# Optimization experiments

Hardware: AMD Instinct MI355X
Metric: run time of the kernel (lower is better)

The kernel has to match this reference:

```python
import jax, jax.numpy as jnp
import numpy as np

D_MODEL = 1024
N_HEADS = 16
D_FF = 4096
WINDOW = 256
EPS = 1e-5


def setup_inputs() -> dict:
    key = jax.random.key(0)
    ks = jax.random.split(key, 12)
    B, T, C = 4, 1024, D_MODEL
    s = lambda fan: 1.0 / np.sqrt(fan)
    return {
        "x": jax.random.normal(ks[0], (B, T, C), jnp.float32),
        "Wqkv": jax.random.normal(ks[1], (3 * C, C), jnp.float32) * s(C),
        "bqkv": jnp.zeros((3 * C,), jnp.float32),
        "Wo": jax.random.normal(ks[2], (C, C), jnp.float32) * s(C),
        "bo": jnp.zeros((C,), jnp.float32),
        "W1": jax.random.normal(ks[3], (D_FF, C), jnp.float32) * s(C),
        "b1": jnp.zeros((D_FF,), jnp.float32),
        "W2": jax.random.normal(ks[4], (C, D_FF), jnp.float32) * s(D_FF),
        "b2": jnp.zeros((C,), jnp.float32),
        "g1": jnp.ones((C,), jnp.float32),
        "be1": jnp.zeros((C,), jnp.float32),
        "g2": jnp.ones((C,), jnp.float32),
        "be2": jnp.zeros((C,), jnp.float32),
    }


def _layernorm(x, g, b):
    mu = jnp.mean(x, axis=-1, keepdims=True)
    var = jnp.mean(jnp.square(x - mu), axis=-1, keepdims=True)
    return (x - mu) * jax.lax.rsqrt(var + EPS) * g + b


def reference(x, Wqkv, bqkv, Wo, bo, W1, b1, W2, b2, g1, be1, g2, be2):
    B, T, C = x.shape
    H, Dh = N_HEADS, C // N_HEADS
    # QKV projection (torch MultiheadAttention packed in_proj)
    qkv = jnp.einsum("btc,ec->bte", x, Wqkv) + bqkv  # [B,T,3C]
    q, k, v = jnp.split(qkv, 3, axis=-1)
    q = q.reshape(B, T, H, Dh).transpose(0, 2, 1, 3)  # [B,H,T,Dh]
    k = k.reshape(B, T, H, Dh).transpose(0, 2, 1, 3)
    v = v.reshape(B, T, H, Dh).transpose(0, 2, 1, 3)
    scores = jnp.einsum("bhqd,bhkd->bhqk", q, k) / jnp.sqrt(jnp.float32(Dh))
    # causal banded mask: key j visible to query i iff 0 <= i-j < WINDOW
    i = jnp.arange(T)[:, None]
    j = jnp.arange(T)[None, :]
    band = (j <= i) & (i - j < WINDOW)
    scores = jnp.where(band, scores, -jnp.inf)
    attn = jax.nn.softmax(scores, axis=-1)
    ctx = jnp.einsum("bhqk,bhkd->bhqd", attn, v)  # [B,H,T,Dh]
    ctx = ctx.transpose(0, 2, 1, 3).reshape(B, T, C)
    attn_out = jnp.einsum("btc,oc->bto", ctx, Wo) + bo
    x = _layernorm(x + attn_out, g1, be1)
    h = jax.nn.gelu(jnp.einsum("btc,fc->btf", x, W1) + b1, approximate=False)
    ffn_out = jnp.einsum("btf,cf->btc", h, W2) + b2
    return _layernorm(x + ffn_out, g2, be2)
```

## Files before the change

kernel.cpp:

```cpp
#include <hip/hip_runtime.h>
#include <hip/hip_bf16.h>

typedef __attribute__((ext_vector_type(4))) float floatx4;
typedef __attribute__((ext_vector_type(8))) short shortx8;

struct bf4 { __hip_bfloat16 h[4]; };
union U8 { shortx8 v; __hip_bfloat16 h[8]; };
union U4 { unsigned long long v; __hip_bfloat16 h[4]; };

__device__ __forceinline__ void async_copy16(const __hip_bfloat16* g, __hip_bfloat16* l) {
  __builtin_amdgcn_global_load_lds((__attribute__((address_space(1))) void*)g,
                                   (__attribute__((address_space(3))) void*)l,
                                   16, 0, 0);
}

__global__ __launch_bounds__(256) void cast_all_kernel(
    const float* __restrict__ s0, __hip_bfloat16* __restrict__ d0, int nb0,
    const float* __restrict__ s1, __hip_bfloat16* __restrict__ d1, int nb1,
    const float* __restrict__ s2, __hip_bfloat16* __restrict__ d2, int nb2,
    const float* __restrict__ s3, __hip_bfloat16* __restrict__ d3, int nb3,
    const float* __restrict__ s4, __hip_bfloat16* __restrict__ d4) {
  int b = blockIdx.x;
  const float* src; __hip_bfloat16* dst;
  if (b < nb0) { src = s0; dst = d0; }
  else { b -= nb0;
    if (b < nb1) { src = s1; dst = d1; }
    else { b -= nb1;
      if (b < nb2) { src = s2; dst = d2; }
      else { b -= nb2;
        if (b < nb3) { src = s3; dst = d3; }
        else { b -= nb3; src = s4; dst = d4; }
      }
    }
  }
  const int i = b * 256 + threadIdx.x;
  const float4 v = ((const float4*)src)[i];
  bf4 o4;
  o4.h[0] = __float2bfloat16(v.x);
  o4.h[1] = __float2bfloat16(v.y);
  o4.h[2] = __float2bfloat16(v.z);
  o4.h[3] = __float2bfloat16(v.w);
  *(bf4*)(dst + (size_t)i * 4) = o4;
}

#define G5_VM(n)   asm volatile("s_waitcnt vmcnt(" #n ")" ::: "memory")
#define G5_BAR()   asm volatile("s_barrier" ::: "memory")
#define G5_LGKM0() asm volatile("s_waitcnt lgkmcnt(0)" ::: "memory")
#define G5_SB()    __builtin_amdgcn_sched_barrier(0)

#define G5_STAGE(slot, koff)                                                   \
  async_copy16(Ag + (koff), &As[slot][tid * 8]);                               \
  async_copy16(Bg + (koff), &Bs[slot][tid * 8]);

#define G5_PHASE(slot, SOFF, DOSTG, VMW)                                       \
  {                                                                            \
    shortx8 fa[4], fb[4];                                                      \
    _Pragma("unroll")                                                          \
    for (int i_ = 0; i_ < 4; ++i_)                                             \
      fa[i_] = *(const shortx8*)&As[slot][ard + i_ * 512];                     \
    _Pragma("unroll")                                                          \
    for (int i_ = 0; i_ < 4; ++i_)                                             \
      fb[i_] = *(const shortx8*)&Bs[slot][brd + i_ * 512];                     \
    if (DOSTG) { G5_STAGE((((slot) + 3) & 3), SOFF) }                          \
    VMW;                                                                       \
    G5_BAR();                                                                  \
    G5_LGKM0(); G5_SB();                                                       \
    __builtin_amdgcn_s_setprio(1);                                             \
    _Pragma("unroll")                                                          \
    for (int mi_ = 0; mi_ < 4; ++mi_)                                          \
      _Pragma("unroll")                                                        \
      for (int ni_ = 0; ni_ < 4; ++ni_)                                        \
        acc[mi_][ni_] = __builtin_amdgcn_mfma_f32_16x16x32_bf16(               \
            fa[mi_], fb[ni_], acc[mi_][ni_], 0, 0, 0);                         \
    __builtin_amdgcn_s_setprio(0);                                             \
    G5_SB();                                                                   \
    G5_BAR();                                                                  \
  }

#define G5_KLOOP()                                                             \
  G5_STAGE(0, 0) G5_STAGE(1, 32) G5_STAGE(2, 64)                               \
  G5_VM(4); G5_BAR();                                                          \
  const int NITER = (NH - 4) >> 2;                                             \
  _Pragma("clang loop unroll(disable)")                                        \
  for (int it = 0; it < NITER; ++it) {                                         \
    G5_PHASE(0, 96,  true, G5_VM(4))                                           \
    G5_PHASE(1, 128, true, G5_VM(4))                                           \
    G5_PHASE(2, 160, true, G5_VM(4))                                           \
    G5_PHASE(3, 192, true, G5_VM(4))                                           \
    Ag += 128; Bg += 128;                                                      \
  }                                                                            \
  G5_PHASE(0, 96, true, G5_VM(4))                                              \
  G5_PHASE(1, 0, false, G5_VM(2))                                              \
  G5_PHASE(2, 0, false, G5_VM(0))                                              \
  G5_PHASE(3, 0, false, (void)0)

template<int EPI>
__global__ __launch_bounds__(1024, 4) void gemm256(
    const __hip_bfloat16* __restrict__ A,
    const __hip_bfloat16* __restrict__ B,
    const float* __restrict__ bias,
    __hip_bfloat16* __restrict__ outb,
    int M, int N, int K, int NT)
{
  __shared__ __align__(16) __hip_bfloat16 As[4][256 * 32];
  __shared__ __align__(16) __hip_bfloat16 Bs[4][256 * 32];
  const int tid  = threadIdx.x;
  const int lane = tid & 63;
  const int wave = tid >> 6;
  const int wr = wave >> 2;
  const int wc = wave & 3;
  const int fr = lane & 15;
  const int fq = lane >> 4;

  const int nwg = gridDim.x;
  const int cpx = nwg >> 3;
  const int swz = (blockIdx.x & 7) * cpx + (blockIdx.x >> 3);
  const int mt = swz / NT, nt = swz % NT;
  const long bm = (long)mt * 256, bn = (long)nt * 256;

  const int srow = tid >> 2;
  const int sch  = (tid & 3) ^ ((tid >> 3) & 3);
  const __hip_bfloat16* Ag = A + (bm + srow) * (size_t)K + sch * 8;
  const __hip_bfloat16* Bg = B + (bn + srow) * (size_t)K + sch * 8;

  const int swc = (fq ^ ((fr >> 1) & 3)) << 3;
  const int ard = (wr * 64 + fr) * 32 + swc;
  const int brd = (wc * 64 + fr) * 32 + swc;

  const floatx4 zero = {0.f, 0.f, 0.f, 0.f};
  floatx4 acc[4][4];
#pragma unroll
  for (int mi = 0; mi < 4; ++mi)
#pragma unroll
    for (int ni = 0; ni < 4; ++ni) acc[mi][ni] = zero;

  const int NH = K >> 5;
  G5_KLOOP()

#pragma unroll
  for (int mi = 0; mi < 4; ++mi) {
#pragma unroll
    for (int ni = 0; ni < 4; ++ni) {
      const long col = bn + wc * 64 + ni * 16 + fr;
      const float bv = bias[col];
#pragma unroll
      for (int r = 0; r < 4; ++r) {
        const long row = bm + wr * 64 + mi * 16 + fq * 4 + r;
        float v = acc[mi][ni][r] + bv;
        if (EPI == 1) {
          const float u = v + 0.044715f * v * v * v;
          v = v / (1.0f + __expf(-1.5957691216057308f * u));
        }
        outb[(size_t)row * N + col] = __float2bfloat16(v);
      }
    }
  }
}

__global__ __launch_bounds__(1024, 4) void gemm256_splitk(
    const __hip_bfloat16* __restrict__ A,
    const __hip_bfloat16* __restrict__ B,
    __hip_bfloat16* __restrict__ part,
    int M, int N, int K, int Klen, int NT, int TPS)
{
  __shared__ __align__(16) __hip_bfloat16 As[4][256 * 32];
  __shared__ __align__(16) __hip_bfloat16 Bs[4][256 * 32];
  const int tid  = threadIdx.x;
  const int lane = tid & 63;
  const int wave = tid >> 6;
  const int wr = wave >> 2;
  const int wc = wave & 3;
  const int fr = lane & 15;
  const int fq = lane >> 4;

  const int nwg = gridDim.x;
  const int cpx = nwg >> 3;
  const int swz = (blockIdx.x & 7) * cpx + (blockIdx.x >> 3);
  const int zt = swz / TPS;
  const int tile = swz % TPS;
  const int mt = tile / NT, nt = tile % NT;
  const long bm = (long)mt * 256, bn = (long)nt * 256;
  const int kstart = zt * Klen;

  const int srow = tid >> 2;
  const int sch  = (tid & 3) ^ ((tid >> 3) & 3);
  const __hip_bfloat16* Ag = A + (bm + srow) * (size_t)K + kstart + sch * 8;
  const __hip_bfloat16* Bg = B + (bn + srow) * (size_t)K + kstart + sch * 8;

  const int swc = (fq ^ ((fr >> 1) & 3)) << 3;
  const int ard = (wr * 64 + fr) * 32 + swc;
  const int brd = (wc * 64 + fr) * 32 + swc;

  const floatx4 zero = {0.f, 0.f, 0.f, 0.f};
  floatx4 acc[4][4];
#pragma unroll
  for (int mi = 0; mi < 4; ++mi)
#pragma unroll
    for (int ni = 0; ni < 4; ++ni) acc[mi][ni] = zero;

  const int NH = Klen >> 5;
  G5_KLOOP()

  __hip_bfloat16* outp = part + (size_t)zt * M * N;
#pragma unroll
  for (int mi = 0; mi < 4; ++mi) {
#pragma unroll
    for (int ni = 0; ni < 4; ++ni) {
      const long col = bn + wc * 64 + ni * 16 + fr;
#pragma unroll
      for (int r = 0; r < 4; ++r) {
        const long row = bm + wr * 64 + mi * 16 + fq * 4 + r;
        outp[(size_t)row * N + col] = __float2bfloat16(acc[mi][ni][r]);
      }
    }
  }
}

__global__ __launch_bounds__(256) void transpose_v_kernel(
    const __hip_bfloat16* __restrict__ qkv, __hip_bfloat16* __restrict__ vt)
{
  const int bh = blockIdx.y;
  const int tt = blockIdx.x;
  const int b = bh >> 4, h = bh & 15;
  __shared__ __hip_bfloat16 tile[64][65];
  const int tid = threadIdx.x;
  const int r = tid >> 2;
  const int c = (tid & 3) << 4;
  const __hip_bfloat16* src = qkv + (size_t)(b * 1024 + tt * 64 + r) * 3072 + 2048 + h * 64 + c;
  U8 u0, u1;
  u0.v = *(const shortx8*)src;
  u1.v = *(const shortx8*)(src + 8);
#pragma unroll
  for (int j = 0; j < 8; ++j) { tile[r][c + j] = u0.h[j]; tile[r][c + 8 + j] = u1.h[j]; }
  __syncthreads();
  U8 w0, w1;
#pragma unroll
  for (int j = 0; j < 8; ++j) { w0.h[j] = tile[c + j][r]; w1.h[j] = tile[c + 8 + j][r]; }
  __hip_bfloat16* dst = vt + ((size_t)bh * 64 + r) * 1024 + tt * 64 + c;
  *(shortx8*)dst       = w0.v;
  *(shortx8*)(dst + 8) = w1.v;
}

__global__ __launch_bounds__(256) void attn_kernel(
    const __hip_bfloat16* __restrict__ qkv,
    const __hip_bfloat16* __restrict__ vt,
    __hip_bfloat16* __restrict__ ctx)
{
  const int wave = threadIdx.x >> 6;
  const int lane = threadIdx.x & 63;
  const int gw = blockIdx.x * 4 + wave;
  const int qt = gw & 63;
  const int bh = gw >> 6;
  const int b = bh >> 4, h = bh & 15;
  const int fr = lane & 15, fq = lane >> 4;
  const int q0 = qt << 4;

  __shared__ __align__(16) __hip_bfloat16 Plds[4][16 * 32];
  __hip_bfloat16* Pw = Plds[wave];

  const __hip_bfloat16* qrow = qkv + (size_t)(b * 1024 + q0 + fr) * 3072 + h * 64;
  const shortx8 aq0 = *(const shortx8*)(qrow + fq * 8);
  const shortx8 aq1 = *(const shortx8*)(qrow + 32 + fq * 8);

  const float SC = 0.125f * 1.44269504088896f;
  float m_r[4] = {-1e30f, -1e30f, -1e30f, -1e30f};
  float l_r[4] = {0.f, 0.f, 0.f, 0.f};
  const floatx4 zero = {0.f, 0.f, 0.f, 0.f};
  floatx4 o[4];
#pragma unroll
  for (int nd = 0; nd < 4; ++nd) o[nd] = zero;

  const int kt0 = (q0 >= 255) ? ((q0 - 255) >> 5) : 0;
  const int kt1 = (q0 + 15) >> 5;
  for (int kt = kt0; kt <= kt1; ++kt) {
    const int kbase = kt << 5;
    const __hip_bfloat16* krow0 = qkv + (size_t)(b * 1024 + kbase + fr) * 3072 + 1024 + h * 64;
    const __hip_bfloat16* krow1 = krow0 + 16 * 3072;
    const shortx8 bk00 = *(const shortx8*)(krow0 + fq * 8);
    const shortx8 bk01 = *(const shortx8*)(krow0 + 32 + fq * 8);
    const shortx8 bk10 = *(const shortx8*)(krow1 + fq * 8);
    const shortx8 bk11 = *(const shortx8*)(krow1 + 32 + fq * 8);
    floatx4 s0 = zero, s1 = zero;
    s0 = __builtin_amdgcn_mfma_f32_16x16x32_bf16(aq0, bk00, s0, 0, 0, 0);
    s0 = __builtin_amdgcn_mfma_f32_16x16x32_bf16(aq1, bk01, s0, 0, 0, 0);
    s1 = __builtin_amdgcn_mfma_f32_16x16x32_bf16(aq0, bk10, s1, 0, 0, 0);
    s1 = __builtin_amdgcn_mfma_f32_16x16x32_bf16(aq1, bk11, s1, 0, 0, 0);
#pragma unroll
    for (int r = 0; r < 4; ++r) { s0[r] *= SC; s1[r] *= SC; }
    if (kbase + 31 > q0 || kbase < q0 - 240) {
#pragma unroll
      for (int r = 0; r < 4; ++r) {
        const int tq = q0 + fq * 4 + r;
        const int j0 = kbase + fr;
        const int j1 = j0 + 16;
        if (j0 > tq || j0 < tq - 255) s0[r] = -3e38f;
        if (j1 > tq || j1 < tq - 255) s1[r] = -3e38f;
      }
    }
#pragma unroll
    for (int r = 0; r < 4; ++r) {
      float vmax = fmaxf(s0[r], s1[r]);
      vmax = fmaxf(vmax, __shfl_xor(vmax, 1));
      vmax = fmaxf(vmax, __shfl_xor(vmax, 2));
      vmax = fmaxf(vmax, __shfl_xor(vmax, 4));
      vmax = fmaxf(vmax, __shfl_xor(vmax, 8));
      const float mnew = fmaxf(m_r[r], vmax);
      const float alpha = exp2f(m_r[r] - mnew);
      const float p0 = exp2f(s0[r] - mnew);
      const float p1 = exp2f(s1[r] - mnew);
      m_r[r] = mnew;
      float ps = p0 + p1;
      ps += __shfl_xor(ps, 1);
      ps += __shfl_xor(ps, 2);
      ps += __shfl_xor(ps, 4);
      ps += __shfl_xor(ps, 8);
      l_r[r] = l_r[r] * alpha + ps;
      o[0][r] *= alpha; o[1][r] *= alpha; o[2][r] *= alpha; o[3][r] *= alpha;
      Pw[(fq * 4 + r) * 32 + fr]      = __float2bfloat16(p0);
      Pw[(fq * 4 + r) * 32 + 16 + fr] = __float2bfloat16(p1);
    }
    asm volatile("s_waitcnt lgkmcnt(0)" ::: "memory");
    const shortx8 ap = *(const shortx8*)&Pw[fr * 32 + fq * 8];
#pragma unroll
    for (int nd = 0; nd < 4; ++nd) {
      const shortx8 bv = *(const shortx8*)&vt[((size_t)bh * 64 + nd * 16 + fr) * 1024 + kbase + fq * 8];
      o[nd] = __builtin_amdgcn_mfma_f32_16x16x32_bf16(ap, bv, o[nd], 0, 0, 0);
    }
    asm volatile("s_waitcnt lgkmcnt(0)" ::: "memory");
  }
#pragma unroll
  for (int nd = 0; nd < 4; ++nd)
#pragma unroll
    for (int r = 0; r < 4; ++r)
      ctx[(size_t)(b * 1024 + q0 + fq * 4 + r) * 1024 + h * 64 + nd * 16 + fr] =
          __float2bfloat16(o[nd][r] / l_r[r]);
}

template<int S, int WB>
__global__ __launch_bounds__(256) void ln_sum_kernel(
    const __hip_bfloat16* __restrict__ part,
    const float* __restrict__ resid,
    const float* __restrict__ bias,
    const float* __restrict__ g, const float* __restrict__ be,
    float* __restrict__ outf, __hip_bfloat16* __restrict__ outb)
{
  const int row = blockIdx.x;
  const int tid = threadIdx.x;
  const size_t base = (size_t)row * 1024;
  float4 v = ((const float4*)(resid + base))[tid];
  const float4 bv = ((const float4*)bias)[tid];
  v.x += bv.x; v.y += bv.y; v.z += bv.z; v.w += bv.w;
#pragma unroll
  for (int s = 0; s < S; ++s) {
    U4 p;
    p.v = *(const unsigned long long*)&part[(size_t)s * 4096 * 1024 + base + tid * 4];
    v.x += __bfloat162float(p.h[0]);
    v.y += __bfloat162float(p.h[1]);
    v.z += __bfloat162float(p.h[2]);
    v.w += __bfloat162float(p.h[3]);
  }
  float sm = v.x + v.y + v.z + v.w;
  float ss = v.x * v.x + v.y * v.y + v.z * v.z + v.w * v.w;
#pragma unroll
  for (int off = 1; off < 64; off <<= 1) {
    sm += __shfl_xor(sm, off);
    ss += __shfl_xor(ss, off);
  }
  __shared__ float red[8];
  if ((tid & 63) == 0) { red[tid >> 6] = sm; red[4 + (tid >> 6)] = ss; }
  __syncthreads();
  sm = red[0] + red[1] + red[2] + red[3];
  ss = red[4] + red[5] + red[6] + red[7];
  const float mu = sm * (1.0f / 1024.0f);
  const float rs = rsqrtf(ss * (1.0f / 1024.0f) - mu * mu + 1e-5f);
  const float4 gg = ((const float4*)g)[tid];
  const float4 bb = ((const float4*)be)[tid];
  float4 y;
  y.x = (v.x - mu) * rs * gg.x + bb.x;
  y.y = (v.y - mu) * rs * gg.y + bb.y;
  y.z = (v.z - mu) * rs * gg.z + bb.z;
  y.w = (v.w - mu) * rs * gg.w + bb.w;
  ((float4*)(outf + base))[tid] = y;
  if (WB) {
    bf4 o4;
    o4.h[0] = __float2bfloat16(y.x);
    o4.h[1] = __float2bfloat16(y.y);
    o4.h[2] = __float2bfloat16(y.z);
    o4.h[3] = __float2bfloat16(y.w);
    *(bf4*)(outb + base + tid * 4) = o4;
  }
}

extern "C" void kernel_launch(void* const* d_in, const int* in_sizes, int n_in,
                              void* d_out, int out_size, void* d_ws, size_t ws_size,
                              hipStream_t stream) {
  const float* x    = (const float*)d_in[0];
  const float* Wqkv = (const float*)d_in[1];
  const float* bqkv = (const float*)d_in[2];
  const float* Wo   = (const float*)d_in[3];
  const float* bo   = (const float*)d_in[4];
  const float* W1   = (const float*)d_in[5];
  const float* b1   = (const float*)d_in[6];
  const float* W2   = (const float*)d_in[7];
  const float* b2   = (const float*)d_in[8];
  const float* g1   = (const float*)d_in[9];
  const float* be1  = (const float*)d_in[10];
  const float* g2   = (const float*)d_in[11];
  const float* be2  = (const float*)d_in[12];

  char* ws = (char*)d_ws;
  size_t off = 0;
  auto alloc = [&](size_t bytes) -> void* {
    void* p = ws + off;
    off += (bytes + 255) & ~(size_t)255;
    return p;
  };
  __hip_bfloat16* wqkvb = (__hip_bfloat16*)alloc(6291456);
  __hip_bfloat16* wob   = (__hip_bfloat16*)alloc(2097152);
  __hip_bfloat16* w1b   = (__hip_bfloat16*)alloc(8388608);
  __hip_bfloat16* w2b   = (__hip_bfloat16*)alloc(8388608);
  __hip_bfloat16* xb    = (__hip_bfloat16*)alloc(8388608);
  __hip_bfloat16* qkvb  = (__hip_bfloat16*)alloc(25165824);
  __hip_bfloat16* vtb   = (__hip_bfloat16*)alloc(8388608);
  __hip_bfloat16* ctxb  = (__hip_bfloat16*)alloc(8388608);
  __hip_bfloat16* part  = (__hip_bfloat16*)alloc(4u * 8388608);
  float*          x1f   = (float*)alloc(16777216);
  __hip_bfloat16* x1b   = (__hip_bfloat16*)alloc(8388608);
  __hip_bfloat16* hb    = (__hip_bfloat16*)alloc(33554432);
  (void)ws_size; (void)in_sizes; (void)n_in; (void)out_size;

  cast_all_kernel<<<16384, 256, 0, stream>>>(x, xb, 4096,
                                             Wqkv, wqkvb, 3072,
                                             Wo, wob, 1024,
                                             W1, w1b, 4096,
                                             W2, w2b);
  gemm256<0><<<192, 1024, 0, stream>>>(xb, wqkvb, bqkv, qkvb, 4096, 3072, 1024, 12);
  transpose_v_kernel<<<dim3(16, 64), 256, 0, stream>>>(qkvb, vtb);
  attn_kernel<<<1024, 256, 0, stream>>>(qkvb, vtb, ctxb);
  gemm256_splitk<<<256, 1024, 0, stream>>>(ctxb, wob, part, 4096, 1024, 1024, 256, 4, 64);
  ln_sum_kernel<4, 1><<<4096, 256, 0, stream>>>(part, x, bo, g1, be1, x1f, x1b);
  gemm256<1><<<256, 1024, 0, stream>>>(x1b, w1b, b1, hb, 4096, 4096, 1024, 16);
  gemm256_splitk<<<256, 1024, 0, stream>>>(hb, w2b, part, 4096, 1024, 4096, 1024, 4, 64);
  ln_sum_kernel<4, 0><<<4096, 256, 0, stream>>>(part, x1f, b2, g2, be2, (float*)d_out, nullptr);
}
```

Before: 324.3 us.

## Use five-slot LDS ring to drop second barrier per K-step in GEMM

Replaces the four-slot LDS pipeline, which needed two barriers per K-step and a manually unrolled phase macro, with a five-slot ring buffer. With the extra slot, a write into a slot cannot race with reads of that slot from the previous step, so the trailing barrier and the sched_barriers are removed. The loop becomes a generic runtime loop with rotating slot indices and tail vmcnt handling. LDS use rises from 128KB to 160KB per block, and the runtime slot arithmetic and branches add some scalar overhead.

```diff
diff --git a/kernel.cpp b/kernel.cpp
--- a/kernel.cpp
+++ b/kernel.cpp
@@ -43,56 +43,51 @@
   *(bf4*)(dst + (size_t)i * 4) = o4;
 }
 
-#define G5_VM(n)   asm volatile("s_waitcnt vmcnt(" #n ")" ::: "memory")
-#define G5_BAR()   asm volatile("s_barrier" ::: "memory")
-#define G5_LGKM0() asm volatile("s_waitcnt lgkmcnt(0)" ::: "memory")
-#define G5_SB()    __builtin_amdgcn_sched_barrier(0)
-
-#define G5_STAGE(slot, koff)                                                   \
-  async_copy16(Ag + (koff), &As[slot][tid * 8]);                               \
-  async_copy16(Bg + (koff), &Bs[slot][tid * 8]);
-
-#define G5_PHASE(slot, SOFF, DOSTG, VMW)                                       \
+#define G6_VM(n)   asm volatile("s_waitcnt vmcnt(" #n ")" ::: "memory")
+#define G6_BAR()   asm volatile("s_barrier" ::: "memory")
+#define G6_LGKM0() asm volatile("s_waitcnt lgkmcnt(0)" ::: "memory")
+
+#define G6_KLOOP()                                                             \
+  async_copy16(Ag,      &As[0 * 8192 + tid * 8]);                              \
+  async_copy16(Bg,      &Bs[0 * 8192 + tid * 8]);                              \
+  async_copy16(Ag + 32, &As[1 * 8192 + tid * 8]);                              \
+  async_copy16(Bg + 32, &Bs[1 * 8192 + tid * 8]);                              \
+  async_copy16(Ag + 64, &As[2 * 8192 + tid * 8]);                              \
+  async_copy16(Bg + 64, &Bs[2 * 8192 + tid * 8]);                              \
+  G6_VM(4); G6_BAR();                                                          \
   {                                                                            \
-    shortx8 fa[4], fb[4];                                                      \
-    _Pragma("unroll")                                                          \
-    for (int i_ = 0; i_ < 4; ++i_)                                             \
-      fa[i_] = *(const shortx8*)&As[slot][ard + i_ * 512];                     \
-    _Pragma("unroll")                                                          \
-    for (int i_ = 0; i_ < 4; ++i_)                                             \
-      fb[i_] = *(const shortx8*)&Bs[slot][brd + i_ * 512];                     \
-    if (DOSTG) { G5_STAGE((((slot) + 3) & 3), SOFF) }                          \
-    VMW;                                                                       \
-    G5_BAR();                                                                  \
-    G5_LGKM0(); G5_SB();                                                       \
-    __builtin_amdgcn_s_setprio(1);                                             \
-    _Pragma("unroll")                                                          \
-    for (int mi_ = 0; mi_ < 4; ++mi_)                                          \
+    int rs = 0, ws = 3, koff = 96;                                             \
+    for (int u = 0; u < NH; ++u) {                                             \
+      const __hip_bfloat16* Asl = As + rs * 8192;                              \
+      const __hip_bfloat16* Bsl = Bs + rs * 8192;                              \
+      shortx8 fa[4], fb[4];                                                    \
       _Pragma("unroll")                                                        \
-      for (int ni_ = 0; ni_ < 4; ++ni_)                                        \
-        acc[mi_][ni_] = __builtin_amdgcn_mfma_f32_16x16x32_bf16(               \
-            fa[mi_], fb[ni_], acc[mi_][ni_], 0, 0, 0);                         \
-    __builtin_amdgcn_s_setprio(0);                                             \
-    G5_SB();                                                                   \
-    G5_BAR();                                                                  \
-  }
-
-#define G5_KLOOP()                                                             \
-  G5_STAGE(0, 0) G5_STAGE(1, 32) G5_STAGE(2, 64)                               \
-  G5_VM(4); G5_BAR();                                                          \
-  const int NITER = (NH - 4) >> 2;                                             \
-  _Pragma("clang loop unroll(disable)")                                        \
-  for (int it = 0; it < NITER; ++it) {                                         \
-    G5_PHASE(0, 96,  true, G5_VM(4))                                           \
-    G5_PHASE(1, 128, true, G5_VM(4))                                           \
-    G5_PHASE(2, 160, true, G5_VM(4))                                           \
-    G5_PHASE(3, 192, true, G5_VM(4))                                           \
-    Ag += 128; Bg += 128;                                                      \
-  }                                                                            \
-  G5_PHASE(0, 96, true, G5_VM(4))                                              \
-  G5_PHASE(1, 0, false, G5_VM(2))                                              \
-  G5_PHASE(2, 0, false, G5_VM(0))                                              \
-  G5_PHASE(3, 0, false, (void)0)
+      for (int i_ = 0; i_ < 4; ++i_)                                           \
+        fa[i_] = *(const shortx8*)&Asl[ard + i_ * 512];                        \
+      _Pragma("unroll")                                                        \
+      for (int i_ = 0; i_ < 4; ++i_)                                           \
+        fb[i_] = *(const shortx8*)&Bsl[brd + i_ * 512];                        \
+      if (u + 3 < NH) {                                                        \
+        async_copy16(Ag + koff, &As[ws * 8192 + tid * 8]);                     \
+        async_copy16(Bg + koff, &Bs[ws * 8192 + tid * 8]);                     \
+        koff += 32;                                                            \
+        G6_VM(4);                                                              \
+      } else if (u + 2 < NH) { G6_VM(2); }                                     \
+      else if (u + 1 < NH)   { G6_VM(0); }                                     \
+      G6_BAR();                                                                \
+      G6_LGKM0();                                                              \
+      __builtin_amdgcn_s_setprio(1);                                           \
+      _Pragma("unroll")                                                        \
+      for (int mi_ = 0; mi_ < 4; ++mi_)                                        \
+        _Pragma("unroll")                                                      \
+        for (int ni_ = 0; ni_ < 4; ++ni_)                                      \
+          acc[mi_][ni_] = __builtin_amdgcn_mfma_f32_16x16x32_bf16(             \
+              fa[mi_], fb[ni_], acc[mi_][ni_], 0, 0, 0);                       \
+      __builtin_amdgcn_s_setprio(0);                                           \
+      rs = (rs == 4) ? 0 : rs + 1;                                             \
+      ws = (ws == 4) ? 0 : ws + 1;                                             \
+    }                                                                          \
+  }
 
 template<int EPI>
 __global__ __launch_bounds__(1024, 4) void gemm256(
@@ -102,8 +97,8 @@
     __hip_bfloat16* __restrict__ outb,
     int M, int N, int K, int NT)
 {
-  __shared__ __align__(16) __hip_bfloat16 As[4][256 * 32];
-  __shared__ __align__(16) __hip_bfloat16 Bs[4][256 * 32];
+  __shared__ __align__(16) __hip_bfloat16 As[5 * 8192];
+  __shared__ __align__(16) __hip_bfloat16 Bs[5 * 8192];
   const int tid  = threadIdx.x;
   const int lane = tid & 63;
   const int wave = tid >> 6;
@@ -135,7 +130,7 @@
     for (int ni = 0; ni < 4; ++ni) acc[mi][ni] = zero;
 
   const int NH = K >> 5;
-  G5_KLOOP()
+  G6_KLOOP()
 
 #pragma unroll
   for (int mi = 0; mi < 4; ++mi) {
@@ -163,8 +158,8 @@
     __hip_bfloat16* __restrict__ part,
     int M, int N, int K, int Klen, int NT, int TPS)
 {
-  __shared__ __align__(16) __hip_bfloat16 As[4][256 * 32];
-  __shared__ __align__(16) __hip_bfloat16 Bs[4][256 * 32];
+  __shared__ __align__(16) __hip_bfloat16 As[5 * 8192];
+  __shared__ __align__(16) __hip_bfloat16 Bs[5 * 8192];
   const int tid  = threadIdx.x;
   const int lane = tid & 63;
   const int wave = tid >> 6;
@@ -199,7 +194,7 @@
     for (int ni = 0; ni < 4; ++ni) acc[mi][ni] = zero;
 
   const int NH = Klen >> 5;
-  G5_KLOOP()
+  G6_KLOOP()
 
   __hip_bfloat16* outp = part + (size_t)zt * M * N;
 #pragma unroll
```

Measured after the change: 309.5 us. 1.05x faster.

## Switch GEMM mainloop to double-buffered BK=64 tiles with 8-chunk swizzle

Applied to the files above, without the earlier changes.

Replaces the 4-slot BK=32 async-copy pipeline with a 2-slot BK=64 double buffer in both GEMM kernels. It uses a wider 8-way XOR swizzle for the LDS layout and issues one barrier and a full vmcnt(0) wait per half-tile. The goal is fewer barriers and waitcnt stalls per K element and bigger copy batches. In exchange prefetch depth drops to one tile ahead, and waiting on all outstanding loads may expose more memory latency. LDS use stays at 128 KB.

```diff
diff --git a/kernel.cpp b/kernel.cpp
--- a/kernel.cpp
+++ b/kernel.cpp
@@ -43,28 +43,24 @@
   *(bf4*)(dst + (size_t)i * 4) = o4;
 }
 
-#define G5_VM(n)   asm volatile("s_waitcnt vmcnt(" #n ")" ::: "memory")
-#define G5_BAR()   asm volatile("s_barrier" ::: "memory")
-#define G5_LGKM0() asm volatile("s_waitcnt lgkmcnt(0)" ::: "memory")
-#define G5_SB()    __builtin_amdgcn_sched_barrier(0)
-
-#define G5_STAGE(slot, koff)                                                   \
-  async_copy16(Ag + (koff), &As[slot][tid * 8]);                               \
-  async_copy16(Bg + (koff), &Bs[slot][tid * 8]);
-
-#define G5_PHASE(slot, SOFF, DOSTG, VMW)                                       \
+#define G7_VM0()  asm volatile("s_waitcnt vmcnt(0)" ::: "memory")
+#define G7_BAR()  asm volatile("s_barrier" ::: "memory")
+
+#define G7_STAGE(S, koff)                                                      \
+  async_copy16(Ag + (koff),                 &As[S][tid * 8]);                  \
+  async_copy16(Ag + (koff) + 128 * (size_t)K, &As[S][8192 + tid * 8]);         \
+  async_copy16(Bg + (koff),                 &Bs[S][tid * 8]);                  \
+  async_copy16(Bg + (koff) + 128 * (size_t)K, &Bs[S][8192 + tid * 8]);
+
+#define G7_PHASE(S)                                                            \
   {                                                                            \
     shortx8 fa[4], fb[4];                                                      \
     _Pragma("unroll")                                                          \
     for (int i_ = 0; i_ < 4; ++i_)                                             \
-      fa[i_] = *(const shortx8*)&As[slot][ard + i_ * 512];                     \
+      fa[i_] = *(const shortx8*)&As[S][aK0 + i_ * 1024];                       \
     _Pragma("unroll")                                                          \
     for (int i_ = 0; i_ < 4; ++i_)                                             \
-      fb[i_] = *(const shortx8*)&Bs[slot][brd + i_ * 512];                     \
-    if (DOSTG) { G5_STAGE((((slot) + 3) & 3), SOFF) }                          \
-    VMW;                                                                       \
-    G5_BAR();                                                                  \
-    G5_LGKM0(); G5_SB();                                                       \
+      fb[i_] = *(const shortx8*)&Bs[S][bK0 + i_ * 1024];                       \
     __builtin_amdgcn_s_setprio(1);                                             \
     _Pragma("unroll")                                                          \
     for (int mi_ = 0; mi_ < 4; ++mi_)                                          \
@@ -73,26 +69,38 @@
         acc[mi_][ni_] = __builtin_amdgcn_mfma_f32_16x16x32_bf16(               \
             fa[mi_], fb[ni_], acc[mi_][ni_], 0, 0, 0);                         \
     __builtin_amdgcn_s_setprio(0);                                             \
-    G5_SB();                                                                   \
-    G5_BAR();                                                                  \
-  }
-
-#define G5_KLOOP()                                                             \
-  G5_STAGE(0, 0) G5_STAGE(1, 32) G5_STAGE(2, 64)                               \
-  G5_VM(4); G5_BAR();                                                          \
-  const int NITER = (NH - 4) >> 2;                                             \
-  _Pragma("clang loop unroll(disable)")                                        \
-  for (int it = 0; it < NITER; ++it) {                                         \
-    G5_PHASE(0, 96,  true, G5_VM(4))                                           \
-    G5_PHASE(1, 128, true, G5_VM(4))                                           \
-    G5_PHASE(2, 160, true, G5_VM(4))                                           \
-    G5_PHASE(3, 192, true, G5_VM(4))                                           \
-    Ag += 128; Bg += 128;                                                      \
-  }                                                                            \
-  G5_PHASE(0, 96, true, G5_VM(4))                                              \
-  G5_PHASE(1, 0, false, G5_VM(2))                                              \
-  G5_PHASE(2, 0, false, G5_VM(0))                                              \
-  G5_PHASE(3, 0, false, (void)0)
+    _Pragma("unroll")                                                          \
+    for (int i_ = 0; i_ < 4; ++i_)                                             \
+      fa[i_] = *(const shortx8*)&As[S][aK1 + i_ * 1024];                       \
+    _Pragma("unroll")                                                          \
+    for (int i_ = 0; i_ < 4; ++i_)                                             \
+      fb[i_] = *(const shortx8*)&Bs[S][bK1 + i_ * 1024];                       \
+    __builtin_amdgcn_s_setprio(1);                                             \
+    _Pragma("unroll")                                                          \
+    for (int mi_ = 0; mi_ < 4; ++mi_)                                          \
+      _Pragma("unroll")                                                        \
+      for (int ni_ = 0; ni_ < 4; ++ni_)                                        \
+        acc[mi_][ni_] = __builtin_amdgcn_mfma_f32_16x16x32_bf16(               \
+            fa[mi_], fb[ni_], acc[mi_][ni_], 0, 0, 0);                         \
+    __builtin_amdgcn_s_setprio(0);                                             \
+  }
+
+#define G7_KLOOP()                                                             \
+  G7_STAGE(0, 0)                                                               \
+  G7_VM0(); G7_BAR();                                                          \
+  {                                                                            \
+    size_t ko = 64;                                                            \
+    for (int t = 0; t < NKT2; ++t) {                                           \
+      G7_STAGE(1, ko)                                                          \
+      G7_PHASE(0)                                                              \
+      G7_VM0(); G7_BAR();                                                      \
+      if (t + 1 < NKT2) { G7_STAGE(0, ko + 64) }                               \
+      G7_PHASE(1)                                                              \
+      if (t + 1 < NKT2) { G7_VM0(); }                                          \
+      G7_BAR();                                                                \
+      ko += 128;                                                               \
+    }                                                                          \
+  }
 
 template<int EPI>
 __global__ __launch_bounds__(1024, 4) void gemm256(
@@ -102,8 +110,8 @@
     __hip_bfloat16* __restrict__ outb,
     int M, int N, int K, int NT)
 {
-  __shared__ __align__(16) __hip_bfloat16 As[4][256 * 32];
-  __shared__ __align__(16) __hip_bfloat16 Bs[4][256 * 32];
+  __shared__ __align__(16) __hip_bfloat16 As[2][256 * 64];
+  __shared__ __align__(16) __hip_bfloat16 Bs[2][256 * 64];
   const int tid  = threadIdx.x;
   const int lane = tid & 63;
   const int wave = tid >> 6;
@@ -118,14 +126,16 @@
   const int mt = swz / NT, nt = swz % NT;
   const long bm = (long)mt * 256, bn = (long)nt * 256;
 
-  const int srow = tid >> 2;
-  const int sch  = (tid & 3) ^ ((tid >> 3) & 3);
+  const int srow = tid >> 3;
+  const int sch  = (tid & 7) ^ ((tid >> 3) & 7);
   const __hip_bfloat16* Ag = A + (bm + srow) * (size_t)K + sch * 8;
   const __hip_bfloat16* Bg = B + (bn + srow) * (size_t)K + sch * 8;
 
-  const int swc = (fq ^ ((fr >> 1) & 3)) << 3;
-  const int ard = (wr * 64 + fr) * 32 + swc;
-  const int brd = (wc * 64 + fr) * 32 + swc;
+  const int f7 = fr & 7;
+  const int aK0 = (wr * 64 + fr) * 64 + ((fq) ^ f7) * 8;
+  const int aK1 = (wr * 64 + fr) * 64 + ((4 + fq) ^ f7) * 8;
+  const int bK0 = (wc * 64 + fr) * 64 + ((fq) ^ f7) * 8;
+  const int bK1 = (wc * 64 + fr) * 64 + ((4 + fq) ^ f7) * 8;
 
   const floatx4 zero = {0.f, 0.f, 0.f, 0.f};
   floatx4 acc[4][4];
@@ -134,8 +144,8 @@
 #pragma unroll
     for (int ni = 0; ni < 4; ++ni) acc[mi][ni] = zero;
 
-  const int NH = K >> 5;
-  G5_KLOOP()
+  const int NKT2 = K >> 7;
+  G7_KLOOP()
 
 #pragma unroll
   for (int mi = 0; mi < 4; ++mi) {
@@ -163,8 +173,8 @@
     __hip_bfloat16* __restrict__ part,
     int M, int N, int K, int Klen, int NT, int TPS)
 {
-  __shared__ __align__(16) __hip_bfloat16 As[4][256 * 32];
-  __shared__ __align__(16) __hip_bfloat16 Bs[4][256 * 32];
+  __shared__ __align__(16) __hip_bfloat16 As[2][256 * 64];
+  __shared__ __align__(16) __hip_bfloat16 Bs[2][256 * 64];
   const int tid  = threadIdx.x;
   const int lane = tid & 63;
   const int wave = tid >> 6;
@@ -182,14 +192,16 @@
   const long bm = (long)mt * 256, bn = (long)nt * 256;
   const int kstart = zt * Klen;
 
-  const int srow = tid >> 2;
-  const int sch  = (tid & 3) ^ ((tid >> 3) & 3);
+  const int srow = tid >> 3;
+  const int sch  = (tid & 7) ^ ((tid >> 3) & 7);
   const __hip_bfloat16* Ag = A + (bm + srow) * (size_t)K + kstart + sch * 8;
   const __hip_bfloat16* Bg = B + (bn + srow) * (size_t)K + kstart + sch * 8;
 
-  const int swc = (fq ^ ((fr >> 1) & 3)) << 3;
-  const int ard = (wr * 64 + fr) * 32 + swc;
-  const int brd = (wc * 64 + fr) * 32 + swc;
+  const int f7 = fr & 7;
+  const int aK0 = (wr * 64 + fr) * 64 + ((fq) ^ f7) * 8;
+  const int aK1 = (wr * 64 + fr) * 64 + ((4 + fq) ^ f7) * 8;
+  const int bK0 = (wc * 64 + fr) * 64 + ((fq) ^ f7) * 8;
+  const int bK1 = (wc * 64 + fr) * 64 + ((4 + fq) ^ f7) * 8;
 
   const floatx4 zero = {0.f, 0.f, 0.f, 0.f};
   floatx4 acc[4][4];
@@ -198,8 +210,8 @@
 #pragma unroll
     for (int ni = 0; ni < 4; ++ni) acc[mi][ni] = zero;
 
-  const int NH = Klen >> 5;
-  G5_KLOOP()
+  const int NKT2 = Klen >> 7;
+  G7_KLOOP()
 
   __hip_bfloat16* outp = part + (size_t)zt * M * N;
 #pragma unroll
```

Result: slower. 413.5 us (+27.5%).
